# Kernel tuning notes

Measured on AMD Instinct MI355X. Metric: run time of the kernel, lower is better.

## Reference

```python
import jax, jax.numpy as jnp
import numpy as np

B, T, D, H = 256, 256, 384, 64  # batch, seq (BLOCK_SIZE), D_MODEL, HEAD_SIZE


def setup_inputs() -> dict:
    key = jax.random.key(0)
    k1, k2, k3, k4 = jax.random.split(key, 4)
    x = jax.random.normal(k1, (B, T, D), dtype=jnp.float32)
    # nn.Linear(D, H, bias=False): weight [H, D]; we store transposed [D, H] for x @ W
    Wq = jax.random.normal(k2, (D, H), dtype=jnp.float32) * (1.0 / np.sqrt(D))
    Wk = jax.random.normal(k3, (D, H), dtype=jnp.float32) * (1.0 / np.sqrt(D))
    Wv = jax.random.normal(k4, (D, H), dtype=jnp.float32) * (1.0 / np.sqrt(D))
    return {"x": x, "Wq": Wq, "Wk": Wk, "Wv": Wv}


def reference(x, Wq, Wk, Wv):
    # x: [B, T, D]
    q = x @ Wq  # [B, T, H]
    k = x @ Wk  # [B, T, H]
    v = x @ Wv  # [B, T, H]
    scale = 1.0 / jnp.sqrt(jnp.asarray(k.shape[-1], dtype=x.dtype))
    wei = jnp.einsum('bth,bsh->bts', q, k) * scale  # [B, T, T]
    causal = jnp.tril(jnp.ones((x.shape[1], x.shape[1]), dtype=bool))
    wei = jnp.where(causal, wei, -jnp.inf)
    wei = jax.nn.softmax(wei, axis=-1)
    # dropout is identity in eval mode (deterministic reference)
    out = jnp.einsum('bts,bsh->bth', wei, v)  # [B, T, H]
    return out
```

## Files before the change

### kernel.cpp

```cpp
#include <hip/hip_runtime.h>

#define BATCH 256
#define TT 256
#define DD 384
#define HH 64
#define SCALE 0.125f
#define SHIFT 14.0f

typedef __attribute__((ext_vector_type(8))) short short8;
typedef __attribute__((ext_vector_type(4))) float floatx4;

#define KS_STRIDE 72
#define QS_STRIDE 72
#define VT_STRIDE 264
#define PS_STRIDE 40
#define WELEMS (3 * DD * HH)

__device__ __forceinline__ unsigned short f2bf(float f) {
    unsigned int u = __float_as_uint(f);
    u += 0x7fffu + ((u >> 16) & 1u);
    return (unsigned short)(u >> 16);
}
__device__ __forceinline__ float bf2f(unsigned short u) {
    return __uint_as_float(((unsigned int)u) << 16);
}

__device__ __forceinline__ void gld_lds16(const void* g, void* ldst) {
    __builtin_amdgcn_global_load_lds(
        (__attribute__((address_space(1))) void*)(unsigned long long)g,
        (__attribute__((address_space(3))) void*)(unsigned int)(unsigned long long)ldst,
        16, 0, 0);
}

__device__ __forceinline__ short8 cvt8(float4 f0, float4 f1) {
    short8 a;
    a[0] = (short)f2bf(f0.x); a[1] = (short)f2bf(f0.y);
    a[2] = (short)f2bf(f0.z); a[3] = (short)f2bf(f0.w);
    a[4] = (short)f2bf(f1.x); a[5] = (short)f2bf(f1.y);
    a[6] = (short)f2bf(f1.z); a[7] = (short)f2bf(f1.w);
    return a;
}

__global__ void pack_w_kernel(const float* __restrict__ wq,
                              const float* __restrict__ wk,
                              const float* __restrict__ wv,
                              unsigned short* __restrict__ wf) {
    int idx = blockIdx.x * 256 + threadIdx.x;
    if (idx >= WELEMS) return;
    int j = idx & 7;
    int lane = (idx >> 3) & 63;
    int nt = (idx >> 9) & 3;
    int rem = idx >> 11;
    int mat = rem % 3;
    int ch = rem / 3;
    int l16 = lane & 15, q = lane >> 4;
    int h = 16 * nt + l16;
    int d = 32 * ch + 8 * q + j;
    const float* w = (mat == 0) ? wq : (mat == 1) ? wk : wv;
    wf[idx] = f2bf(w[d * HH + h]);
}

__global__ __launch_bounds__(512, 2)
void fused_kernel(const float* __restrict__ x, const unsigned short* __restrict__ wfrag,
                  float* __restrict__ out) {
    __shared__ __align__(16) union LdsU {
        unsigned short w[WELEMS];
        struct {
            unsigned short ks[TT * KS_STRIDE];
            unsigned short vt[HH * VT_STRIDE];
            unsigned short q[TT * QS_STRIDE];
            unsigned short p[8][16 * PS_STRIDE];
        } s;
    } U;

    const int b = blockIdx.x;
    const int tid = threadIdx.x;
    const int wave = tid >> 6;
    const int lane = tid & 63;
    const int quad = lane >> 4;
    const int l16 = lane & 15;

    const float* xb = x + (size_t)b * TT * DD;

    const float* xr0 = xb + (size_t)(32 * wave + l16) * DD + 8 * quad;
    const float* xr1 = xr0 + (size_t)16 * DD;

    floatx4 cq[2][4] = {};
    floatx4 ck[2][4] = {};
    floatx4 cv[2][4] = {};

    float4 xfA[4], xfB[4];

    xfA[0] = *(const float4*)(xr0);
    xfA[1] = *(const float4*)(xr0 + 4);
    xfA[2] = *(const float4*)(xr1);
    xfA[3] = *(const float4*)(xr1 + 4);

    #pragma unroll
    for (int t = 0; t < 18; ++t) {
        int grp = wave * 18 + t;
        gld_lds16(wfrag + (size_t)grp * 512 + lane * 8, U.w + grp * 512);
    }

    __syncthreads();

    #define GEMM_BODY(CUR, NXT, CH, PREF)                                          \
        {                                                                          \
            if (PREF) {                                                            \
                const float* p0_ = xr0 + ((CH) + 1) * 32;                          \
                const float* p1_ = xr1 + ((CH) + 1) * 32;                          \
                NXT[0] = *(const float4*)(p0_);                                    \
                NXT[1] = *(const float4*)(p0_ + 4);                                \
                NXT[2] = *(const float4*)(p1_);                                    \
                NXT[3] = *(const float4*)(p1_ + 4);                                \
            }                                                                      \
            short8 wf_[12];                                                        \
            _Pragma("unroll")                                                      \
            for (int i = 0; i < 12; ++i)                                           \
                wf_[i] = *(const short8*)(U.w + (size_t)((CH) * 12 + i) * 512 + lane * 8); \
            short8 a0 = cvt8(CUR[0], CUR[1]);                                      \
            short8 a1 = cvt8(CUR[2], CUR[3]);                                      \
            _Pragma("unroll")                                                      \
            for (int nt = 0; nt < 4; ++nt) {                                       \
                cq[0][nt] = __builtin_amdgcn_mfma_f32_16x16x32_bf16(a0, wf_[nt], cq[0][nt], 0, 0, 0);      \
                cq[1][nt] = __builtin_amdgcn_mfma_f32_16x16x32_bf16(a1, wf_[nt], cq[1][nt], 0, 0, 0);      \
                ck[0][nt] = __builtin_amdgcn_mfma_f32_16x16x32_bf16(a0, wf_[4 + nt], ck[0][nt], 0, 0, 0);  \
                ck[1][nt] = __builtin_amdgcn_mfma_f32_16x16x32_bf16(a1, wf_[4 + nt], ck[1][nt], 0, 0, 0);  \
                cv[0][nt] = __builtin_amdgcn_mfma_f32_16x16x32_bf16(a0, wf_[8 + nt], cv[0][nt], 0, 0, 0);  \
                cv[1][nt] = __builtin_amdgcn_mfma_f32_16x16x32_bf16(a1, wf_[8 + nt], cv[1][nt], 0, 0, 0);  \
            }                                                                      \
        }

    #pragma unroll 1
    for (int t = 0; t < 6; ++t) {
        GEMM_BODY(xfA, xfB, 2 * t, 1);
        GEMM_BODY(xfB, xfA, 2 * t + 1, (t < 5));
    }
    #undef GEMM_BODY

    __syncthreads();

    #pragma unroll
    for (int mi = 0; mi < 2; ++mi)
      #pragma unroll
      for (int nt = 0; nt < 4; ++nt)
        #pragma unroll
        for (int r = 0; r < 4; ++r) {
            int row = 32 * wave + 16 * mi + 4 * quad + r;
            int col = 16 * nt + l16;
            U.s.q[row * QS_STRIDE + col] = f2bf(cq[mi][nt][r]);
            U.s.ks[row * KS_STRIDE + col] = f2bf(ck[mi][nt][r]);
            U.s.vt[col * VT_STRIDE + row] = f2bf(cv[mi][nt][r]);
        }

    __syncthreads();

    floatx4 o[2][4] = {};
    float l_run[2][4] = {{0.f, 0.f, 0.f, 0.f}, {0.f, 0.f, 0.f, 0.f}};
    unsigned short* psw = U.s.p[wave];

    #pragma unroll
    for (int gi = 0; gi < 2; ++gi) {
        int g = gi ? (15 - wave) : wave;
        int gr0 = 16 * g;
        short8 aq0 = *(const short8*)(U.s.q + (size_t)(gr0 + l16) * QS_STRIDE + quad * 8);
        short8 aq1 = *(const short8*)(U.s.q + (size_t)(gr0 + l16) * QS_STRIDE + 32 + quad * 8);
        int clast = g >> 1;
        for (int c = 0; c <= clast; ++c) {
            floatx4 s[2] = {};
            #pragma unroll
            for (int ni = 0; ni < 2; ++ni) {
                const unsigned short* kbase =
                    U.s.ks + (size_t)(32 * c + 16 * ni + l16) * KS_STRIDE + quad * 8;
                s[ni] = __builtin_amdgcn_mfma_f32_16x16x32_bf16(aq0, *(const short8*)(kbase), s[ni], 0, 0, 0);
                s[ni] = __builtin_amdgcn_mfma_f32_16x16x32_bf16(aq1, *(const short8*)(kbase + 32), s[ni], 0, 0, 0);
            }
            bool partial = (c == clast);
            #pragma unroll
            for (int r = 0; r < 4; ++r) {
                int row = gr0 + 4 * quad + r;
                float p0 = __expf(s[0][r] * SCALE - SHIFT);
                float p1 = __expf(s[1][r] * SCALE - SHIFT);
                if (partial) {
                    if (32 * c + l16 > row) p0 = 0.f;
                    if (32 * c + 16 + l16 > row) p1 = 0.f;
                }
                unsigned short b0 = f2bf(p0), b1 = f2bf(p1);
                l_run[gi][r] += bf2f(b0) + bf2f(b1);
                psw[(4 * quad + r) * PS_STRIDE + l16] = b0;
                psw[(4 * quad + r) * PS_STRIDE + 16 + l16] = b1;
            }
            short8 ap = *(const short8*)(psw + l16 * PS_STRIDE + quad * 8);
            #pragma unroll
            for (int nt = 0; nt < 4; ++nt) {
                short8 bv = *(const short8*)(U.s.vt + (size_t)(16 * nt + l16) * VT_STRIDE + 32 * c + quad * 8);
                o[gi][nt] = __builtin_amdgcn_mfma_f32_16x16x32_bf16(ap, bv, o[gi][nt], 0, 0, 0);
            }
        }
    }

    float* outb = out + (size_t)b * TT * HH;
    #pragma unroll
    for (int gi = 0; gi < 2; ++gi) {
        int g = gi ? (15 - wave) : wave;
        #pragma unroll
        for (int r = 0; r < 4; ++r) {
            float l = l_run[gi][r];
            l += __shfl_xor(l, 1);
            l += __shfl_xor(l, 2);
            l += __shfl_xor(l, 4);
            l += __shfl_xor(l, 8);
            l_run[gi][r] = l;
        }
        #pragma unroll
        for (int nt = 0; nt < 4; ++nt)
          #pragma unroll
          for (int r = 0; r < 4; ++r) {
            int row = 16 * g + 4 * quad + r;
            outb[(size_t)row * HH + 16 * nt + l16] = o[gi][nt][r] / l_run[gi][r];
          }
    }
}

extern "C" void kernel_launch(void* const* d_in, const int* in_sizes, int n_in,
                              void* d_out, int out_size, void* d_ws, size_t ws_size,
                              hipStream_t stream) {
    const float* x  = (const float*)d_in[0];
    const float* wq = (const float*)d_in[1];
    const float* wk = (const float*)d_in[2];
    const float* wv = (const float*)d_in[3];
    unsigned short* wf = (unsigned short*)d_ws;
    float* o = (float*)d_out;

    pack_w_kernel<<<(WELEMS + 255) / 256, 256, 0, stream>>>(wq, wk, wv, wf);
    fused_kernel<<<BATCH, 512, 0, stream>>>(x, wf, o);
}
```

Measured before the change: 169.1 us.

## Deepen x prefetch to four chunks, permute K layout, and use reciprocal normalization

```diff
diff --git a/kernel.cpp b/kernel.cpp
--- a/kernel.cpp
+++ b/kernel.cpp
@@ -55,7 +55,7 @@
     int ch = rem / 3;
     int l16 = lane & 15, q = lane >> 4;
     int h = 16 * nt + l16;
-    int d = 32 * ch + 8 * q + j;
+    int d = 32 * ch + 4 * q + (j < 4 ? j : j + 12);
     const float* w = (mat == 0) ? wq : (mat == 1) ? wk : wv;
     wf[idx] = f2bf(w[d * HH + h]);
 }
@@ -82,19 +82,28 @@
 
     const float* xb = x + (size_t)b * TT * DD;
 
-    const float* xr0 = xb + (size_t)(32 * wave + l16) * DD + 8 * quad;
+    const float* xr0 = xb + (size_t)(32 * wave + l16) * DD + 4 * quad;
     const float* xr1 = xr0 + (size_t)16 * DD;
 
     floatx4 cq[2][4] = {};
     floatx4 ck[2][4] = {};
     floatx4 cv[2][4] = {};
 
-    float4 xfA[4], xfB[4];
-
-    xfA[0] = *(const float4*)(xr0);
-    xfA[1] = *(const float4*)(xr0 + 4);
-    xfA[2] = *(const float4*)(xr1);
-    xfA[3] = *(const float4*)(xr1 + 4);
+    float4 xP0_0, xP0_1, xP0_2, xP0_3;
+    float4 xP1_0, xP1_1, xP1_2, xP1_3;
+    float4 xP2_0, xP2_1, xP2_2, xP2_3;
+    float4 xP3_0, xP3_1, xP3_2, xP3_3;
+
+    #define XLOAD(B, CH)                                   \
+        B##_0 = *(const float4*)(xr0 + (CH) * 32);         \
+        B##_1 = *(const float4*)(xr0 + (CH) * 32 + 16);    \
+        B##_2 = *(const float4*)(xr1 + (CH) * 32);         \
+        B##_3 = *(const float4*)(xr1 + (CH) * 32 + 16);
+
+    XLOAD(xP0, 0)
+    XLOAD(xP1, 1)
+    XLOAD(xP2, 2)
+    XLOAD(xP3, 3)
 
     #pragma unroll
     for (int t = 0; t < 18; ++t) {
@@ -104,22 +113,16 @@
 
     __syncthreads();
 
-    #define GEMM_BODY(CUR, NXT, CH, PREF)                                          \
+    #define GEMM_BODY(B, CH)                                                       \
         {                                                                          \
-            if (PREF) {                                                            \
-                const float* p0_ = xr0 + ((CH) + 1) * 32;                          \
-                const float* p1_ = xr1 + ((CH) + 1) * 32;                          \
-                NXT[0] = *(const float4*)(p0_);                                    \
-                NXT[1] = *(const float4*)(p0_ + 4);                                \
-                NXT[2] = *(const float4*)(p1_);                                    \
-                NXT[3] = *(const float4*)(p1_ + 4);                                \
-            }                                                                      \
+            short8 a0 = cvt8(B##_0, B##_1);                                        \
+            short8 a1 = cvt8(B##_2, B##_3);                                        \
+            if ((CH) + 4 < 12) { XLOAD(B, (CH) + 4) }                              \
+            const unsigned short* wb = U.w + (size_t)(CH) * 12 * 512 + lane * 8;   \
             short8 wf_[12];                                                        \
             _Pragma("unroll")                                                      \
             for (int i = 0; i < 12; ++i)                                           \
-                wf_[i] = *(const short8*)(U.w + (size_t)((CH) * 12 + i) * 512 + lane * 8); \
-            short8 a0 = cvt8(CUR[0], CUR[1]);                                      \
-            short8 a1 = cvt8(CUR[2], CUR[3]);                                      \
+                wf_[i] = *(const short8*)(wb + (size_t)i * 512);                   \
             _Pragma("unroll")                                                      \
             for (int nt = 0; nt < 4; ++nt) {                                       \
                 cq[0][nt] = __builtin_amdgcn_mfma_f32_16x16x32_bf16(a0, wf_[nt], cq[0][nt], 0, 0, 0);      \
@@ -131,12 +134,20 @@
             }                                                                      \
         }
 
-    #pragma unroll 1
-    for (int t = 0; t < 6; ++t) {
-        GEMM_BODY(xfA, xfB, 2 * t, 1);
-        GEMM_BODY(xfB, xfA, 2 * t + 1, (t < 5));
-    }
+    GEMM_BODY(xP0, 0)
+    GEMM_BODY(xP1, 1)
+    GEMM_BODY(xP2, 2)
+    GEMM_BODY(xP3, 3)
+    GEMM_BODY(xP0, 4)
+    GEMM_BODY(xP1, 5)
+    GEMM_BODY(xP2, 6)
+    GEMM_BODY(xP3, 7)
+    GEMM_BODY(xP0, 8)
+    GEMM_BODY(xP1, 9)
+    GEMM_BODY(xP2, 10)
+    GEMM_BODY(xP3, 11)
     #undef GEMM_BODY
+    #undef XLOAD
 
     __syncthreads();
 
@@ -203,6 +214,7 @@
     #pragma unroll
     for (int gi = 0; gi < 2; ++gi) {
         int g = gi ? (15 - wave) : wave;
+        float linv[4];
         #pragma unroll
         for (int r = 0; r < 4; ++r) {
             float l = l_run[gi][r];
@@ -210,14 +222,14 @@
             l += __shfl_xor(l, 2);
             l += __shfl_xor(l, 4);
             l += __shfl_xor(l, 8);
-            l_run[gi][r] = l;
+            linv[r] = 1.0f / l;
         }
         #pragma unroll
         for (int nt = 0; nt < 4; ++nt)
           #pragma unroll
           for (int r = 0; r < 4; ++r) {
             int row = 16 * g + 4 * quad + r;
-            outb[(size_t)row * HH + 16 * nt + l16] = o[gi][nt][r] / l_run[gi][r];
+            outb[(size_t)row * HH + 16 * nt + l16] = o[gi][nt][r] * linv[r];
           }
     }
 }
```

Measured after the change: 171.2 us. About the same (+1.3%).
